# Kernel tuning notes

Measured on AMD Instinct MI355X. Metric: run time of the kernel, lower is better.

The kernel has to match this reference:

```python
import jax, jax.numpy as jnp
import numpy as np

K_KNN = 20
TC = 3  # taylor_channel
N_TERMS = 20  # trivariate polynomial terms up to order 3
CHANNELS = [(6, 32), (32, 64), (64, 128), (128, 256)]


def _knn_indices(xyz, k):
    sq = jnp.sum(xyz * xyz, axis=1)  # B x N
    d2 = sq[:, :, None] + sq[:, None, :] - 2.0 * jnp.einsum('bci,bcj->bij', xyz, xyz)
    _, idx = jax.lax.top_k(-d2, k)
    return idx


def _group(feat, idx):
    # feat: B x C x N, idx: B x N x K -> B x C x N x K
    return jax.vmap(lambda f, i: f[:, i])(feat, idx)


def _taylor_terms(g):
    X, Y, Z = g[:, 0], g[:, 1], g[:, 2]
    one = jnp.ones_like(X)
    terms = [one, X, Y, Z, X * Y, X * Z, Y * Z, X * X, Y * Y, Z * Z,
             X * X * Y, X * X * Z, X * Y * Y, Y * Y * Z, X * Z * Z, Y * Z * Z,
             X * Y * Z, X * X * X, Y * Y * Y, Z * Z * Z]
    return jnp.stack(terms, axis=1)


def _spider_conv(feat, idx, terms, w1, b1, w2, b2):
    # feat: B x C x N; w1: tc x 20; w2: out x (C*tc) x K
    B, C, N = feat.shape
    g = _group(feat, idx)  # B x C x N x K
    taylor = jnp.einsum('btnk,ot->bonk', terms, w1) + b1[None, :, None, None]
    g = (g[:, :, None, :, :] * taylor[:, None, :, :, :]).reshape(B, C * TC, N, g.shape[-1])
    out = jnp.einsum('bcnk,ock->bon', g, w2) + b2[None, :, None]
    return jax.nn.relu(out)


def _forward(pc, params):
    # pc: B x N x 6
    pcT = jnp.transpose(pc, (0, 2, 1))
    xyz = pcT[:, 0:3, :]
    idx = _knn_indices(xyz, K_KNN)  # B x N x K
    grouped_xyz = _group(xyz, idx)
    grouped_pc = grouped_xyz - xyz[:, :, :, None]  # relative coords
    terms = _taylor_terms(grouped_pc)
    feat = pcT
    feats = []
    for l in range(4):
        w1, b1, w2, b2 = params[l]
        feat = _spider_conv(feat, idx, terms, w1, b1, w2, b2)
        feats.append(feat)
    cat = jnp.concatenate(feats, axis=1)
    top2, _ = jax.lax.top_k(cat, 2)  # topk over point dim (last axis)
    return top2.reshape(cat.shape[0], -1)  # B x 960


def setup_inputs() -> dict:
    key = jax.random.key(0)
    keys = jax.random.split(key, 1 + 16)
    B, N = 4, 2048
    inp = {'pc': jax.random.normal(keys[0], (B, N, 6), dtype=jnp.float32)}
    ki = 1
    for l, (cin, cout) in enumerate(CHANNELS):
        inp[f'w1_{l}'] = jax.random.normal(keys[ki], (TC, N_TERMS), dtype=jnp.float32) * 0.1; ki += 1
        inp[f'b1_{l}'] = jax.random.normal(keys[ki], (TC,), dtype=jnp.float32) * 0.01; ki += 1
        inp[f'w2_{l}'] = jax.random.normal(keys[ki], (cout, cin * TC, K_KNN), dtype=jnp.float32) * (1.0 / np.sqrt(cin * TC * K_KNN)); ki += 1
        inp[f'b2_{l}'] = jax.random.normal(keys[ki], (cout,), dtype=jnp.float32) * 0.01; ki += 1
    return inp


def reference(pc, w1_0, b1_0, w2_0, b2_0, w1_1, b1_1, w2_1, b2_1,
              w1_2, b1_2, w2_2, b2_2, w1_3, b1_3, w2_3, b2_3):
    params = [(w1_0, b1_0, w2_0, b2_0), (w1_1, b1_1, w2_1, b2_1),
              (w1_2, b1_2, w2_2, b2_2), (w1_3, b1_3, w2_3, b2_3)]
    return _forward(pc, params)
```

## Files before the change

kernel.cpp:

```cpp
#include <hip/hip_runtime.h>
#include <math.h>

#define BB 4
#define NN 2048
#define KNN 20

typedef _Float16 f16x8 __attribute__((ext_vector_type(8)));
typedef _Float16 f16x4 __attribute__((ext_vector_type(4)));
typedef _Float16 f16x2 __attribute__((ext_vector_type(2)));
typedef float f32x4 __attribute__((ext_vector_type(4)));

#define DPP_STEP(CTRL, RMASK)                                                   \
    {                                                                           \
        unsigned ov = (unsigned)__builtin_amdgcn_update_dpp(                    \
            (int)bv, (int)bv, CTRL, RMASK, 0xf, false);                         \
        unsigned oj = (unsigned)__builtin_amdgcn_update_dpp(                    \
            (int)jj, (int)jj, CTRL, RMASK, 0xf, false);                         \
        bool lt = (ov < bv) || (ov == bv && oj < jj);                           \
        bv = lt ? ov : bv;                                                      \
        jj = lt ? oj : jj;                                                      \
    }

__global__ __launch_bounds__(256) void knn_kernel(const float* __restrict__ pc,
                                                  int* __restrict__ idx_out,
                                                  float* __restrict__ rel_out) {
    __shared__ float4 sp[NN];
    const int tid = threadIdx.x;
    const int b = blockIdx.x / (NN / 4);
    const int grp = blockIdx.x % (NN / 4);
    for (int p = tid; p < NN; p += 256) {
        float x = pc[(size_t)(b * NN + p) * 6 + 0];
        float y = pc[(size_t)(b * NN + p) * 6 + 1];
        float z = pc[(size_t)(b * NN + p) * 6 + 2];
        float4 v;
        v.x = x; v.y = y; v.z = z;
        v.w = __fadd_rn(__fadd_rn(__fmul_rn(x, x), __fmul_rn(y, y)), __fmul_rn(z, z));
        sp[p] = v;
    }
    __syncthreads();
    const int lane = tid & 63;
    const int i = grp * 4 + (tid >> 6);
    const float4 pi = sp[i];
    const float xi = pi.x, yi = pi.y, zi = pi.z, sqi = pi.w;

    unsigned mmr[32];
#pragma unroll
    for (int t = 0; t < 32; ++t) {
        const int j = t * 64 + lane;
        const float4 pj = sp[j];
        float dot = __fadd_rn(__fadd_rn(__fmul_rn(xi, pj.x), __fmul_rn(yi, pj.y)),
                              __fmul_rn(zi, pj.z));
        float d2 = __fsub_rn(__fadd_rn(sqi, pj.w), __fmul_rn(2.0f, dot));
        unsigned bbits = __float_as_uint(d2);
        mmr[t] = bbits ^ (0x80000000u | (unsigned)((int)bbits >> 31));
    }

    const unsigned UMAX = 0xFFFFFFFFu;
    unsigned mask = 0u;
    unsigned v1, t1, v2, t2;

    auto refill = [&]() {
        v1 = UMAX; t1 = 0u; v2 = UMAX; t2 = 0u;
#pragma unroll
        for (int t = 0; t < 32; ++t) {
            unsigned m = ((mask >> t) & 1u) ? UMAX : mmr[t];
            bool c1 = m < v1;
            bool c2 = m < v2;
            unsigned nv2 = c1 ? v1 : (c2 ? m : v2);
            unsigned nt2 = c1 ? t1 : (c2 ? (unsigned)t : t2);
            v1 = c1 ? m : v1;
            t1 = c1 ? (unsigned)t : t1;
            v2 = nv2; t2 = nt2;
        }
    };
    refill();

    const size_t orow = (size_t)(b * NN + i);
    for (int k = 0; k < KNN; ++k) {
        unsigned bv = v1;
        unsigned jj = (t1 << 6) | (unsigned)lane;
        DPP_STEP(0x111, 0xf)
        DPP_STEP(0x112, 0xf)
        DPP_STEP(0x114, 0xf)
        DPP_STEP(0x118, 0xf)
        DPP_STEP(0x142, 0xa)
        DPP_STEP(0x143, 0xc)
        const unsigned sj = (unsigned)__builtin_amdgcn_readlane((int)jj, 63);
        if (lane == 0) {
            idx_out[orow * KNN + k] = (int)sj;
            const float4 pj = sp[sj];
            size_t ro = (orow * KNN + k) * 3;
            rel_out[ro + 0] = __fsub_rn(pj.x, xi);
            rel_out[ro + 1] = __fsub_rn(pj.y, yi);
            rel_out[ro + 2] = __fsub_rn(pj.z, zi);
        }
        if (k < KNN - 1) {
            bool am = ((sj & 63u) == (unsigned)lane);
            if (am) {
                mask |= (1u << (sj >> 6));
                v1 = v2; t1 = t2; v2 = UMAX;
            }
            if (__ballot(v1 == UMAX) != 0ull) refill();
        }
    }
}

__global__ __launch_bounds__(256) void taylor_all_kernel(
    const float* __restrict__ rel,
    const float* __restrict__ w10, const float* __restrict__ b10, _Float16* __restrict__ ty0,
    const float* __restrict__ w11, const float* __restrict__ b11, _Float16* __restrict__ ty1,
    const float* __restrict__ w12, const float* __restrict__ b12, _Float16* __restrict__ ty2,
    const float* __restrict__ w13, const float* __restrict__ b13, _Float16* __restrict__ ty3) {
    __shared__ float w1s[4][60];
    __shared__ float b1s[4][3];
    const int tid = threadIdx.x;
    if (tid < 240) {
        const float* wp = (tid < 60) ? w10 : (tid < 120) ? w11 : (tid < 180) ? w12 : w13;
        w1s[tid / 60][tid % 60] = wp[tid % 60];
    } else if (tid < 252) {
        int r = tid - 240;
        const float* bp = (r < 3) ? b10 : (r < 6) ? b11 : (r < 9) ? b12 : b13;
        b1s[r / 3][r % 3] = bp[r % 3];
    }
    __syncthreads();
    int t = blockIdx.x * 256 + tid;
    if (t >= BB * NN * KNN) return;
    float X = rel[(size_t)t * 3 + 0], Y = rel[(size_t)t * 3 + 1], Z = rel[(size_t)t * 3 + 2];
    float tm[20];
    tm[0] = 1.f; tm[1] = X; tm[2] = Y; tm[3] = Z;
    tm[4] = X * Y; tm[5] = X * Z; tm[6] = Y * Z;
    tm[7] = X * X; tm[8] = Y * Y; tm[9] = Z * Z;
    tm[10] = X * X * Y; tm[11] = X * X * Z; tm[12] = X * Y * Y; tm[13] = Y * Y * Z;
    tm[14] = X * Z * Z; tm[15] = Y * Z * Z; tm[16] = X * Y * Z;
    tm[17] = X * X * X; tm[18] = Y * Y * Y; tm[19] = Z * Z * Z;
    _Float16* typ[4] = {ty0, ty1, ty2, ty3};
#pragma unroll
    for (int l = 0; l < 4; ++l) {
#pragma unroll
        for (int o = 0; o < 3; ++o) {
            float a = b1s[l][o];
#pragma unroll
            for (int q = 0; q < 20; ++q) a += w1s[l][o * 20 + q] * tm[q];
            typ[l][(size_t)t * 3 + o] = (_Float16)a;
        }
    }
}

struct WsplitArgs {
    const float* w2[4];
    _Float16* wf[4];
    int COUT[4], CIN[4], CPAD[4], OCB[4], KCB[4];
    int cum[4];
};

__global__ __launch_bounds__(256) void wsplit_all_kernel(WsplitArgs a) {
    int e = blockIdx.x * 256 + threadIdx.x;
    if (e >= a.cum[3]) return;
    int l = (e >= a.cum[0]) + (e >= a.cum[1]) + (e >= a.cum[2]);
    int base = l ? a.cum[l - 1] : 0;
    e -= base;
    const int KCB = a.KCB[l], OCB = a.OCB[l], CPAD = a.CPAD[l], CIN = a.CIN[l];
    int i = e & 7;
    int lane = (e >> 3) & 63;
    int fi = e >> 9;
    int kcb = fi % KCB;
    int ocb = (fi / KCB) % OCB;
    int k = fi / (KCB * OCB);
    int oc = ocb * 16 + (lane & 15);
    int kk = kcb * 32 + (lane >> 4) * 8 + i;
    int o = kk / CPAD, c = kk % CPAD;
    float x = 0.f;
    if (o < 3 && c < CIN)
        x = a.w2[l][((size_t)oc * (CIN * 3) + c * 3 + o) * KNN + k];
    a.wf[l][e] = (_Float16)x;
}

template <int CIN, int COUT, int CK3P, int NT, int WM, int WN, int FM, int FN,
          int OCT, int KSPLIT, bool L0S>
__global__ __launch_bounds__(256) void convm_kernel(const float* __restrict__ fin,
                                                    const int* __restrict__ idx,
                                                    const _Float16* __restrict__ tyg,
                                                    const _Float16* __restrict__ wf,
                                                    float* __restrict__ out) {
    constexpr int KR = KNN / KSPLIT;
    constexpr int SR = CK3P + 8;
    constexpr int KCB = CK3P / 32;
    constexpr int OCB = COUT / 16;
    constexpr int OCBLK = WM * FM * 16;
    constexpr int NTL = NN / NT;
    constexpr int TPR = 256 / NT;
    constexpr int CT = L0S ? 6 : (CIN / TPR);
    constexpr int CQ = L0S ? 2 : (CT / 4);
    static_assert(WN * FN * 16 == NT, "n tiling");
    static_assert(OCBLK * OCT == COUT, "oc tiling");
    static_assert(WM * WN == 4, "4 waves");

    __shared__ _Float16 Bs[NT * SR];
    __shared__ _Float16 tyt[NT][3 * KR];
    __shared__ int idxt[NT][KR];

    const int tid = threadIdx.x;
    const int lane = tid & 63;
    const int wid = tid >> 6;
    const int wm = wid / WN;
    const int wn = wid % WN;
    int t = blockIdx.x;
    const int ks = t % KSPLIT; t /= KSPLIT;
    const int oct = t % OCT;   t /= OCT;
    const int ntl = t % NTL;   t /= NTL;
    const int b = t;
    const int n0 = ntl * NT;
    const int oc0 = oct * OCBLK;
    const int k0 = ks * KR;
    const size_t brow = (size_t)b * NN;

    for (int e = tid; e < NT * KR; e += 256) {
        int n = e / KR, kk = e % KR;
        idxt[n][kk] = idx[(brow + n0 + n) * KNN + k0 + kk];
    }
    for (int e = tid; e < NT * 3 * KR; e += 256) {
        int n = e / (3 * KR), q = e % (3 * KR);
        tyt[n][q] = tyg[((brow + n0 + n) * KNN + k0) * 3 + q];
    }
    __syncthreads();

    const int nrow = tid & 63;
    const int sub = tid >> 6;
    float4 g[CQ];

    auto issue_gather = [&](int kk) {
        if constexpr (L0S) {
            if (tid < 192) {
                int j = idxt[nrow][kk];
                const float* p = fin + (brow + j) * 6;
                g[0] = *reinterpret_cast<const float4*>(p);
                float2 r2 = *reinterpret_cast<const float2*>(p + 4);
                g[1].x = r2.x; g[1].y = r2.y;
            }
        } else {
            int j = idxt[nrow][kk];
            const float* p = fin + (brow + j) * CIN + sub * CT;
#pragma unroll
            for (int q = 0; q < CQ; ++q)
                g[q] = *reinterpret_cast<const float4*>(p + q * 4);
        }
    };
    issue_gather(0);

    f32x4 acc[FM][FN];
#pragma unroll
    for (int fm = 0; fm < FM; ++fm)
#pragma unroll
        for (int fn = 0; fn < FN; ++fn) acc[fm][fn] = (f32x4){0.f, 0.f, 0.f, 0.f};

    f16x8 areg[FM * KCB];
    auto loadA_burst = [&](int k) {
#pragma unroll
        for (int fm = 0; fm < FM; ++fm)
#pragma unroll
            for (int kcb = 0; kcb < KCB; ++kcb) {
                size_t fidx = ((size_t)k * OCB + (oc0 >> 4) + wm * FM + fm) * KCB + kcb;
                areg[fm * KCB + kcb] =
                    *reinterpret_cast<const f16x8*>(&wf[(fidx * 64 + lane) * 8]);
            }
    };

    for (int kk = 0; kk < KR; ++kk) {
        const int k = k0 + kk;
        loadA_burst(k);
        __syncthreads();
        if constexpr (L0S) {
            if (tid < 192) {
                _Float16 th = tyt[nrow][kk * 3 + sub];
                f16x2 tb; tb[0] = th; tb[1] = th;
                f16x2 g0, g1, g2;
                g0[0] = (_Float16)g[0].x; g0[1] = (_Float16)g[0].y;
                g1[0] = (_Float16)g[0].z; g1[1] = (_Float16)g[0].w;
                g2[0] = (_Float16)g[1].x; g2[1] = (_Float16)g[1].y;
                f16x2 p0 = g0 * tb, p1 = g1 * tb, p2 = g2 * tb;
                f16x8 hv;
                hv[0] = p0[0]; hv[1] = p0[1]; hv[2] = p1[0]; hv[3] = p1[1];
                hv[4] = p2[0]; hv[5] = p2[1]; hv[6] = (_Float16)0.f; hv[7] = (_Float16)0.f;
                *reinterpret_cast<f16x8*>(&Bs[nrow * SR + sub * 8]) = hv;
                if (sub == 0) {
                    f16x8 z = {};
                    *reinterpret_cast<f16x8*>(&Bs[nrow * SR + 24]) = z;
                }
            }
        } else {
            f16x2 gh[CT / 2];
#pragma unroll
            for (int q = 0; q < CQ; ++q) {
                f16x2 a0, a1;
                a0[0] = (_Float16)g[q].x; a0[1] = (_Float16)g[q].y;
                a1[0] = (_Float16)g[q].z; a1[1] = (_Float16)g[q].w;
                gh[2 * q] = a0; gh[2 * q + 1] = a1;
            }
            _Float16 th0 = tyt[nrow][kk * 3 + 0];
            _Float16 th1 = tyt[nrow][kk * 3 + 1];
            _Float16 th2 = tyt[nrow][kk * 3 + 2];
#pragma unroll
            for (int o = 0; o < 3; ++o) {
                _Float16 th = (o == 0) ? th0 : (o == 1) ? th1 : th2;
                f16x2 tb; tb[0] = th; tb[1] = th;
#pragma unroll
                for (int qp = 0; qp < CT / 8; ++qp) {
                    f16x2 p0 = gh[4 * qp + 0] * tb;
                    f16x2 p1 = gh[4 * qp + 1] * tb;
                    f16x2 p2 = gh[4 * qp + 2] * tb;
                    f16x2 p3 = gh[4 * qp + 3] * tb;
                    f16x8 hv;
                    hv[0] = p0[0]; hv[1] = p0[1]; hv[2] = p1[0]; hv[3] = p1[1];
                    hv[4] = p2[0]; hv[5] = p2[1]; hv[6] = p3[0]; hv[7] = p3[1];
                    *reinterpret_cast<f16x8*>(
                        &Bs[nrow * SR + o * CIN + sub * CT + qp * 8]) = hv;
                }
            }
        }
        __syncthreads();
        if (kk + 1 < KR) issue_gather(kk + 1);
#pragma unroll
        for (int kcb = 0; kcb < KCB; ++kcb) {
            f16x8 bf[FN];
#pragma unroll
            for (int fn = 0; fn < FN; ++fn) {
                int row = wn * FN * 16 + fn * 16 + (lane & 15);
                bf[fn] = *reinterpret_cast<const f16x8*>(
                    &Bs[row * SR + kcb * 32 + (lane >> 4) * 8]);
            }
#pragma unroll
            for (int fm = 0; fm < FM; ++fm)
#pragma unroll
                for (int fn = 0; fn < FN; ++fn)
                    acc[fm][fn] = __builtin_amdgcn_mfma_f32_16x16x32_f16(
                        areg[fm * KCB + kcb], bf[fn], acc[fm][fn], 0, 0, 0);
        }
    }
    float* dst = out + (size_t)ks * ((size_t)BB * NN * COUT);
#pragma unroll
    for (int fm = 0; fm < FM; ++fm) {
        const int ocb = oc0 + wm * FM * 16 + fm * 16 + ((lane >> 4) << 2);
#pragma unroll
        for (int fn = 0; fn < FN; ++fn) {
            int n = n0 + wn * FN * 16 + fn * 16 + (lane & 15);
            float4 o4;
            o4.x = acc[fm][fn][0]; o4.y = acc[fm][fn][1];
            o4.z = acc[fm][fn][2]; o4.w = acc[fm][fn][3];
            *reinterpret_cast<float4*>(&dst[(brow + n) * COUT + ocb]) = o4;
        }
    }
}

template <int COUT, int KS>
__global__ __launch_bounds__(256) void combine_kernel(const float* __restrict__ p,
                                                      const float* __restrict__ b2,
                                                      float* __restrict__ out) {
    constexpr size_t TOT = (size_t)BB * NN * COUT;
    size_t i = (size_t)blockIdx.x * 256 + threadIdx.x;
    if (i * 4 >= TOT) return;
    const float4* p4 = reinterpret_cast<const float4*>(p);
    float4 a = p4[i];
#pragma unroll
    for (int s = 1; s < KS; ++s) {
        float4 v = p4[i + s * (TOT / 4)];
        a.x += v.x; a.y += v.y; a.z += v.z; a.w += v.w;
    }
    float4 bb = *reinterpret_cast<const float4*>(&b2[(i * 4) % COUT]);
    float4 r;
    r.x = fmaxf(a.x + bb.x, 0.f); r.y = fmaxf(a.y + bb.y, 0.f);
    r.z = fmaxf(a.z + bb.z, 0.f); r.w = fmaxf(a.w + bb.w, 0.f);
    reinterpret_cast<float4*>(out)[i] = r;
}

__global__ __launch_bounds__(256) void top2_kernel(const float* __restrict__ f1,
                                                   const float* __restrict__ f2,
                                                   const float* __restrict__ f3,
                                                   const float* __restrict__ p3,
                                                   const float* __restrict__ b23,
                                                   float* __restrict__ out) {
    __shared__ float m1s[256], m2s[256];
    const int bid = blockIdx.x;
    const int b = bid / 480;
    const int ch = bid % 480;
    const size_t brow = (size_t)b * NN;
    float m1 = -INFINITY, m2 = -INFINITY;
    if (ch < 224) {
        const float* f; int C, c;
        if (ch < 32)       { f = f1; C = 32;  c = ch; }
        else if (ch < 96)  { f = f2; C = 64;  c = ch - 32; }
        else               { f = f3; C = 128; c = ch - 96; }
        for (int n = threadIdx.x; n < NN; n += 256) {
            float v = f[(brow + n) * C + c];
            if (v > m1) { m2 = m1; m1 = v; }
            else if (v > m2) m2 = v;
        }
    } else {
        const int c = ch - 224;
        const float bc = b23[c];
        constexpr size_t TOT3 = (size_t)BB * NN * 256;
        for (int n = threadIdx.x; n < NN; n += 256) {
            size_t o = (brow + n) * 256 + c;
            float v = fmaxf(p3[o] + p3[TOT3 + o] + bc, 0.f);
            if (v > m1) { m2 = m1; m1 = v; }
            else if (v > m2) m2 = v;
        }
    }
    m1s[threadIdx.x] = m1; m2s[threadIdx.x] = m2;
    __syncthreads();
    for (int s = 128; s > 0; s >>= 1) {
        if (threadIdx.x < s) {
            float a1 = m1s[threadIdx.x], a2 = m2s[threadIdx.x];
            float c1 = m1s[threadIdx.x + s], c2 = m2s[threadIdx.x + s];
            m1s[threadIdx.x] = fmaxf(a1, c1);
            m2s[threadIdx.x] = fmaxf(fminf(a1, c1), fmaxf(a2, c2));
        }
        __syncthreads();
    }
    if (threadIdx.x == 0) {
        out[(size_t)b * 960 + ch * 2 + 0] = m1s[0];
        out[(size_t)b * 960 + ch * 2 + 1] = m2s[0];
    }
}

extern "C" void kernel_launch(void* const* d_in, const int* in_sizes, int n_in,
                              void* d_out, int out_size, void* d_ws, size_t ws_size,
                              hipStream_t stream) {
    const float* pc = (const float*)d_in[0];
    const float *w1[4], *b1[4], *w2[4], *b2[4];
    for (int l = 0; l < 4; ++l) {
        w1[l] = (const float*)d_in[1 + 4 * l];
        b1[l] = (const float*)d_in[2 + 4 * l];
        w2[l] = (const float*)d_in[3 + 4 * l];
        b2[l] = (const float*)d_in[4 + 4 * l];
    }
    char* ws = (char*)d_ws;
    size_t off = 0;
    auto alloc = [&](size_t bytes) -> void* {
        void* p = ws + off;
        off = (off + bytes + 255) & ~(size_t)255;
        return p;
    };
    int* idxb      = (int*)alloc((size_t)BB * NN * KNN * 4);
    float* rel     = (float*)alloc((size_t)BB * NN * KNN * 3 * 4);
    _Float16* ty0  = (_Float16*)alloc((size_t)BB * NN * KNN * 3 * 2);
    _Float16* ty1  = (_Float16*)alloc((size_t)BB * NN * KNN * 3 * 2);
    _Float16* ty2  = (_Float16*)alloc((size_t)BB * NN * KNN * 3 * 2);
    _Float16* ty3  = (_Float16*)alloc((size_t)BB * NN * KNN * 3 * 2);
    const int wtot0 = KNN * 2 * 1 * 512;
    const int wtot1 = KNN * 4 * 3 * 512;
    const int wtot2 = KNN * 8 * 6 * 512;
    const int wtot3 = KNN * 16 * 12 * 512;
    _Float16* wf0 = (_Float16*)alloc((size_t)wtot0 * 2);
    _Float16* wf1 = (_Float16*)alloc((size_t)wtot1 * 2);
    _Float16* wf2 = (_Float16*)alloc((size_t)wtot2 * 2);
    _Float16* wf3 = (_Float16*)alloc((size_t)wtot3 * 2);
    float* f1     = (float*)alloc((size_t)BB * NN * 32 * 4);
    float* f2     = (float*)alloc((size_t)BB * NN * 64 * 4);
    float* f3     = (float*)alloc((size_t)BB * NN * 128 * 4);
    float* pbuf   = (float*)alloc((size_t)4 * BB * NN * 128 * 4);

    knn_kernel<<<BB * NN / 4, 256, 0, stream>>>(pc, idxb, rel);

    taylor_all_kernel<<<(BB * NN * KNN + 255) / 256, 256, 0, stream>>>(
        rel, w1[0], b1[0], ty0, w1[1], b1[1], ty1, w1[2], b1[2], ty2, w1[3], b1[3], ty3);

    WsplitArgs wa;
    wa.w2[0] = w2[0]; wa.w2[1] = w2[1]; wa.w2[2] = w2[2]; wa.w2[3] = w2[3];
    wa.wf[0] = wf0; wa.wf[1] = wf1; wa.wf[2] = wf2; wa.wf[3] = wf3;
    int COUTs[4] = {32, 64, 128, 256}, CINs[4] = {6, 32, 64, 128};
    int CPADs[4] = {8, 32, 64, 128}, OCBs[4] = {2, 4, 8, 16}, KCBs[4] = {1, 3, 6, 12};
    int cum = 0;
    for (int l = 0; l < 4; ++l) {
        wa.COUT[l] = COUTs[l]; wa.CIN[l] = CINs[l]; wa.CPAD[l] = CPADs[l];
        wa.OCB[l] = OCBs[l]; wa.KCB[l] = KCBs[l];
        cum += KNN * OCBs[l] * KCBs[l] * 512;
        wa.cum[l] = cum;
    }
    wsplit_all_kernel<<<(cum + 255) / 256, 256, 0, stream>>>(wa);

    convm_kernel<6, 32, 32, 64, 2, 2, 1, 2, 1, 4, true>
        <<<512, 256, 0, stream>>>(pc, idxb, ty0, wf0, pbuf);
    combine_kernel<32, 4><<<(BB * NN * 32 / 4 + 255) / 256, 256, 0, stream>>>(pbuf, b2[0], f1);

    convm_kernel<32, 64, 96, 64, 4, 1, 1, 4, 1, 4, false>
        <<<512, 256, 0, stream>>>(f1, idxb, ty1, wf1, pbuf);
    combine_kernel<64, 4><<<(BB * NN * 64 / 4 + 255) / 256, 256, 0, stream>>>(pbuf, b2[1], f2);

    convm_kernel<64, 128, 192, 64, 4, 1, 2, 4, 1, 4, false>
        <<<512, 256, 0, stream>>>(f2, idxb, ty2, wf2, pbuf);
    combine_kernel<128, 4><<<(BB * NN * 128 / 4 + 255) / 256, 256, 0, stream>>>(pbuf, b2[2], f3);

    convm_kernel<128, 256, 384, 64, 4, 1, 2, 4, 2, 2, false>
        <<<512, 256, 0, stream>>>(f3, idxb, ty3, wf3, pbuf);

    top2_kernel<<<BB * 480, 256, 0, stream>>>(f1, f2, f3, pbuf, b2[3], (float*)d_out);
}
```

Before: 191.0 us.

## Split layer-4 reduction dim into halves, raise K-split and occupancy

Adds a HALVES template parameter so the conv kernel stages its shared-memory B tile and A-register burst over half the reduction width at a time. This cuts LDS footprint and register count, and launch_bounds now requests 3 blocks per CU. Layer 4 also moves to a 4-way neighbor split with twice the blocks, so the partial buffer grows and top2 sums four partials. The aim is more occupancy and parallelism for the largest layer, at the cost of extra barriers per neighbor and more partial-sum traffic.

```diff
diff --git a/kernel.cpp b/kernel.cpp
--- a/kernel.cpp
+++ b/kernel.cpp
@@ -175,16 +175,18 @@
     a.wf[l][e] = (_Float16)x;
 }
 
-template <int CIN, int COUT, int CK3P, int NT, int WM, int WN, int FM, int FN,
-          int OCT, int KSPLIT, bool L0S>
-__global__ __launch_bounds__(256) void convm_kernel(const float* __restrict__ fin,
-                                                    const int* __restrict__ idx,
-                                                    const _Float16* __restrict__ tyg,
-                                                    const _Float16* __restrict__ wf,
-                                                    float* __restrict__ out) {
+template <int CIN, int COUT, int CK3P, int HALVES, int NT, int WM, int WN,
+          int FM, int FN, int OCT, int KSPLIT, bool L0S>
+__global__ __launch_bounds__(256, 3) void convm_kernel(const float* __restrict__ fin,
+                                                       const int* __restrict__ idx,
+                                                       const _Float16* __restrict__ tyg,
+                                                       const _Float16* __restrict__ wf,
+                                                       float* __restrict__ out) {
     constexpr int KR = KNN / KSPLIT;
-    constexpr int SR = CK3P + 8;
+    constexpr int CKH = CK3P / HALVES;
+    constexpr int SR = CKH + 8;
     constexpr int KCB = CK3P / 32;
+    constexpr int KCBH = CKH / 32;
     constexpr int OCB = COUT / 16;
     constexpr int OCBLK = WM * FM * 16;
     constexpr int NTL = NN / NT;
@@ -194,6 +196,7 @@
     static_assert(WN * FN * 16 == NT, "n tiling");
     static_assert(OCBLK * OCT == COUT, "oc tiling");
     static_assert(WM * WN == 4, "4 waves");
+    static_assert(!L0S || HALVES == 1, "L0S single-half");
 
     __shared__ _Float16 Bs[NT * SR];
     __shared__ _Float16 tyt[NT][3 * KR];
@@ -253,42 +256,27 @@
 #pragma unroll
         for (int fn = 0; fn < FN; ++fn) acc[fm][fn] = (f32x4){0.f, 0.f, 0.f, 0.f};
 
-    f16x8 areg[FM * KCB];
-    auto loadA_burst = [&](int k) {
+    f16x8 areg[FM * KCBH];
+    auto loadA_burst = [&](int k, int h) {
 #pragma unroll
         for (int fm = 0; fm < FM; ++fm)
 #pragma unroll
-            for (int kcb = 0; kcb < KCB; ++kcb) {
-                size_t fidx = ((size_t)k * OCB + (oc0 >> 4) + wm * FM + fm) * KCB + kcb;
-                areg[fm * KCB + kcb] =
+            for (int kcb = 0; kcb < KCBH; ++kcb) {
+                size_t fidx = ((size_t)k * OCB + (oc0 >> 4) + wm * FM + fm) * KCB +
+                              h * KCBH + kcb;
+                areg[fm * KCBH + kcb] =
                     *reinterpret_cast<const f16x8*>(&wf[(fidx * 64 + lane) * 8]);
             }
     };
 
     for (int kk = 0; kk < KR; ++kk) {
         const int k = k0 + kk;
-        loadA_burst(k);
-        __syncthreads();
+        f16x2 gh[L0S ? 3 : (CT / 2)];
         if constexpr (L0S) {
-            if (tid < 192) {
-                _Float16 th = tyt[nrow][kk * 3 + sub];
-                f16x2 tb; tb[0] = th; tb[1] = th;
-                f16x2 g0, g1, g2;
-                g0[0] = (_Float16)g[0].x; g0[1] = (_Float16)g[0].y;
-                g1[0] = (_Float16)g[0].z; g1[1] = (_Float16)g[0].w;
-                g2[0] = (_Float16)g[1].x; g2[1] = (_Float16)g[1].y;
-                f16x2 p0 = g0 * tb, p1 = g1 * tb, p2 = g2 * tb;
-                f16x8 hv;
-                hv[0] = p0[0]; hv[1] = p0[1]; hv[2] = p1[0]; hv[3] = p1[1];
-                hv[4] = p2[0]; hv[5] = p2[1]; hv[6] = (_Float16)0.f; hv[7] = (_Float16)0.f;
-                *reinterpret_cast<f16x8*>(&Bs[nrow * SR + sub * 8]) = hv;
-                if (sub == 0) {
-                    f16x8 z = {};
-                    *reinterpret_cast<f16x8*>(&Bs[nrow * SR + 24]) = z;
-                }
-            }
+            gh[0][0] = (_Float16)g[0].x; gh[0][1] = (_Float16)g[0].y;
+            gh[1][0] = (_Float16)g[0].z; gh[1][1] = (_Float16)g[0].w;
+            gh[2][0] = (_Float16)g[1].x; gh[2][1] = (_Float16)g[1].y;
         } else {
-            f16x2 gh[CT / 2];
 #pragma unroll
             for (int q = 0; q < CQ; ++q) {
                 f16x2 a0, a1;
@@ -296,44 +284,67 @@
                 a1[0] = (_Float16)g[q].z; a1[1] = (_Float16)g[q].w;
                 gh[2 * q] = a0; gh[2 * q + 1] = a1;
             }
-            _Float16 th0 = tyt[nrow][kk * 3 + 0];
-            _Float16 th1 = tyt[nrow][kk * 3 + 1];
-            _Float16 th2 = tyt[nrow][kk * 3 + 2];
-#pragma unroll
-            for (int o = 0; o < 3; ++o) {
-                _Float16 th = (o == 0) ? th0 : (o == 1) ? th1 : th2;
-                f16x2 tb; tb[0] = th; tb[1] = th;
-#pragma unroll
-                for (int qp = 0; qp < CT / 8; ++qp) {
-                    f16x2 p0 = gh[4 * qp + 0] * tb;
-                    f16x2 p1 = gh[4 * qp + 1] * tb;
-                    f16x2 p2 = gh[4 * qp + 2] * tb;
-                    f16x2 p3 = gh[4 * qp + 3] * tb;
+        }
+        _Float16 th0 = tyt[nrow][kk * 3 + 0];
+        _Float16 th1 = tyt[nrow][kk * 3 + 1];
+        _Float16 th2 = tyt[nrow][kk * 3 + 2];
+#pragma unroll
+        for (int h = 0; h < HALVES; ++h) {
+            loadA_burst(k, h);
+            __syncthreads();
+            if constexpr (L0S) {
+                if (tid < 192) {
+                    _Float16 th = tyt[nrow][kk * 3 + sub];
+                    f16x2 tb; tb[0] = th; tb[1] = th;
+                    f16x2 p0 = gh[0] * tb, p1 = gh[1] * tb, p2 = gh[2] * tb;
                     f16x8 hv;
                     hv[0] = p0[0]; hv[1] = p0[1]; hv[2] = p1[0]; hv[3] = p1[1];
-                    hv[4] = p2[0]; hv[5] = p2[1]; hv[6] = p3[0]; hv[7] = p3[1];
-                    *reinterpret_cast<f16x8*>(
-                        &Bs[nrow * SR + o * CIN + sub * CT + qp * 8]) = hv;
+                    hv[4] = p2[0]; hv[5] = p2[1]; hv[6] = (_Float16)0.f; hv[7] = (_Float16)0.f;
+                    *reinterpret_cast<f16x8*>(&Bs[nrow * SR + sub * 8]) = hv;
+                    if (sub == 0) {
+                        f16x8 z = {};
+                        *reinterpret_cast<f16x8*>(&Bs[nrow * SR + 24]) = z;
+                    }
+                }
+            } else {
+#pragma unroll
+                for (int o = 0; o < 3; ++o) {
+                    const int kkpos = o * CIN + sub * CT;
+                    if (kkpos / CKH != h) continue;
+                    _Float16 th = (o == 0) ? th0 : (o == 1) ? th1 : th2;
+                    f16x2 tb; tb[0] = th; tb[1] = th;
+#pragma unroll
+                    for (int qp = 0; qp < CT / 8; ++qp) {
+                        f16x2 p0 = gh[4 * qp + 0] * tb;
+                        f16x2 p1 = gh[4 * qp + 1] * tb;
+                        f16x2 p2 = gh[4 * qp + 2] * tb;
+                        f16x2 p3 = gh[4 * qp + 3] * tb;
+                        f16x8 hv;
+                        hv[0] = p0[0]; hv[1] = p0[1]; hv[2] = p1[0]; hv[3] = p1[1];
+                        hv[4] = p2[0]; hv[5] = p2[1]; hv[6] = p3[0]; hv[7] = p3[1];
+                        *reinterpret_cast<f16x8*>(
+                            &Bs[nrow * SR + (kkpos - h * CKH) + qp * 8]) = hv;
+                    }
                 }
             }
-        }
-        __syncthreads();
-        if (kk + 1 < KR) issue_gather(kk + 1);
-#pragma unroll
-        for (int kcb = 0; kcb < KCB; ++kcb) {
-            f16x8 bf[FN];
-#pragma unroll
-            for (int fn = 0; fn < FN; ++fn) {
-                int row = wn * FN * 16 + fn * 16 + (lane & 15);
-                bf[fn] = *reinterpret_cast<const f16x8*>(
-                    &Bs[row * SR + kcb * 32 + (lane >> 4) * 8]);
+            __syncthreads();
+            if (h == HALVES - 1 && kk + 1 < KR) issue_gather(kk + 1);
+#pragma unroll
+            for (int kcb = 0; kcb < KCBH; ++kcb) {
+                f16x8 bf[FN];
+#pragma unroll
+                for (int fn = 0; fn < FN; ++fn) {
+                    int row = wn * FN * 16 + fn * 16 + (lane & 15);
+                    bf[fn] = *reinterpret_cast<const f16x8*>(
+                        &Bs[row * SR + kcb * 32 + (lane >> 4) * 8]);
+                }
+#pragma unroll
+                for (int fm = 0; fm < FM; ++fm)
+#pragma unroll
+                    for (int fn = 0; fn < FN; ++fn)
+                        acc[fm][fn] = __builtin_amdgcn_mfma_f32_16x16x32_f16(
+                            areg[fm * KCBH + kcb], bf[fn], acc[fm][fn], 0, 0, 0);
             }
-#pragma unroll
-            for (int fm = 0; fm < FM; ++fm)
-#pragma unroll
-                for (int fn = 0; fn < FN; ++fn)
-                    acc[fm][fn] = __builtin_amdgcn_mfma_f32_16x16x32_f16(
-                        areg[fm * KCB + kcb], bf[fn], acc[fm][fn], 0, 0, 0);
         }
     }
     float* dst = out + (size_t)ks * ((size_t)BB * NN * COUT);
@@ -400,7 +411,7 @@
         constexpr size_t TOT3 = (size_t)BB * NN * 256;
         for (int n = threadIdx.x; n < NN; n += 256) {
             size_t o = (brow + n) * 256 + c;
-            float v = fmaxf(p3[o] + p3[TOT3 + o] + bc, 0.f);
+            float v = fmaxf(p3[o] + p3[TOT3 + o] + p3[2 * TOT3 + o] + p3[3 * TOT3 + o] + bc, 0.f);
             if (v > m1) { m2 = m1; m1 = v; }
             else if (v > m2) m2 = v;
         }
@@ -457,7 +468,7 @@
     float* f1     = (float*)alloc((size_t)BB * NN * 32 * 4);
     float* f2     = (float*)alloc((size_t)BB * NN * 64 * 4);
     float* f3     = (float*)alloc((size_t)BB * NN * 128 * 4);
-    float* pbuf   = (float*)alloc((size_t)4 * BB * NN * 128 * 4);
+    float* pbuf   = (float*)alloc((size_t)4 * BB * NN * 256 * 4);
 
     knn_kernel<<<BB * NN / 4, 256, 0, stream>>>(pc, idxb, rel);
 
@@ -478,20 +489,20 @@
     }
     wsplit_all_kernel<<<(cum + 255) / 256, 256, 0, stream>>>(wa);
 
-    convm_kernel<6, 32, 32, 64, 2, 2, 1, 2, 1, 4, true>
+    convm_kernel<6, 32, 32, 1, 64, 2, 2, 1, 2, 1, 4, true>
         <<<512, 256, 0, stream>>>(pc, idxb, ty0, wf0, pbuf);
     combine_kernel<32, 4><<<(BB * NN * 32 / 4 + 255) / 256, 256, 0, stream>>>(pbuf, b2[0], f1);
 
-    convm_kernel<32, 64, 96, 64, 4, 1, 1, 4, 1, 4, false>
+    convm_kernel<32, 64, 96, 1, 64, 4, 1, 1, 4, 1, 4, false>
         <<<512, 256, 0, stream>>>(f1, idxb, ty1, wf1, pbuf);
     combine_kernel<64, 4><<<(BB * NN * 64 / 4 + 255) / 256, 256, 0, stream>>>(pbuf, b2[1], f2);
 
-    convm_kernel<64, 128, 192, 64, 4, 1, 2, 4, 1, 4, false>
+    convm_kernel<64, 128, 192, 1, 64, 4, 1, 2, 4, 1, 4, false>
         <<<512, 256, 0, stream>>>(f2, idxb, ty2, wf2, pbuf);
     combine_kernel<128, 4><<<(BB * NN * 128 / 4 + 255) / 256, 256, 0, stream>>>(pbuf, b2[2], f3);
 
-    convm_kernel<128, 256, 384, 64, 4, 1, 2, 4, 2, 2, false>
-        <<<512, 256, 0, stream>>>(f3, idxb, ty3, wf3, pbuf);
+    convm_kernel<128, 256, 384, 2, 64, 4, 1, 2, 4, 2, 4, false>
+        <<<1024, 256, 0, stream>>>(f3, idxb, ty3, wf3, pbuf);
 
     top2_kernel<<<BB * 480, 256, 0, stream>>>(f1, f2, f3, pbuf, b2[3], (float*)d_out);
 }
```

Result: slower. 261.8 us (+37.0%).
